# Kernel optimization log

Hardware: AMD Instinct MI355X
Metric: run time of the kernel (lower is better)

## Reference

```python
import jax, jax.numpy as jnp
import numpy as np

NUM_CLASSES = 151  # Visual Genome object classes
PRED_DIM = 51      # predicate distribution channels (50 predicates + bg)


def _conv2d(x, w, pad):
    # x: [B, Cin, H, W], w: [Cout, Cin, kh, kw]
    return jax.lax.conv_general_dilated(
        x, w, window_strides=(1, 1), padding=[(pad, pad), (pad, pad)],
        dimension_numbers=("NCHW", "OIHW", "NCHW"))


def setup_inputs() -> dict:
    key = jax.random.key(0)
    ks = jax.random.split(key, 12)
    B, N, D = 64, 80, 4096
    K = D // 4  # 1024
    s = 0.02
    return {
        "encoder_reps": jax.random.normal(ks[0], (B, N, D), jnp.float32),
        "obj_preds": jax.random.randint(ks[1], (B, N), 0, NUM_CLASSES, jnp.int32),
        "freq_table": jax.random.normal(ks[2], (NUM_CLASSES * NUM_CLASSES, PRED_DIM), jnp.float32),
        "W_comp": jax.random.normal(ks[3], (D, K), jnp.float32) * s,
        "W_ou1": jax.random.normal(ks[4], (K, K), jnp.float32) * s,
        "W_ofc": jax.random.normal(ks[5], (K, K), jnp.float32) * s,
        "W_decomp": jax.random.normal(ks[6], (K, D), jnp.float32) * s,
        "conv1": jax.random.normal(ks[7], (10, PRED_DIM, 3, 3), jnp.float32) * s,
        "conv2": jax.random.normal(ks[8], (5, 10, 3, 3), jnp.float32) * s,
        "conv3": jax.random.normal(ks[9], (1, 5, 1, 1), jnp.float32) * s,
    }


def reference(encoder_reps, obj_preds, freq_table, W_comp, W_ou1, W_ofc,
              W_decomp, conv1, conv2, conv3):
    B, N, D = encoder_reps.shape
    # obj_comp: Linear(D, D//4, bias=False) + ReLU
    comp = jax.nn.relu(jnp.einsum("bnd,dk->bnk", encoder_reps, W_comp))  # [B,N,K]
    # ou1: Linear(K, K, bias=False) + ReLU
    obj_u1 = jax.nn.relu(jnp.einsum("bnk,kj->bnj", comp, W_ou1))          # [B,N,K]
    # pairwise product indices -> freq_bias.index_with_labels (subj*C + obj)
    pair_idx = obj_preds[:, :, None] * NUM_CLASSES + obj_preds[:, None, :]  # [B,N,N]
    rel_u1 = freq_table[pair_idx]                                          # [B,N,N,51]
    # adjacency via small conv stack + sigmoid
    x = jnp.transpose(rel_u1, (0, 3, 1, 2))      # [B,51,N,N]
    x = _conv2d(x, conv1, pad=1)                 # [B,10,N,N]
    x = _conv2d(x, conv2, pad=1)                 # [B,5,N,N]
    x = _conv2d(x, conv3, pad=0)                 # [B,1,N,N]
    adj = jax.nn.sigmoid(x[:, 0])                # [B,N,N]
    # normalized Laplacian: D^-1/2 (A + I) D^-1/2
    A_hat = adj + jnp.eye(N, dtype=adj.dtype)[None]
    d = (jnp.sum(A_hat, axis=2) + 1e-5) ** (-0.5)                          # [B,N]
    L_hat = d[:, :, None] * A_hat * d[:, None, :]                          # [B,N,N]
    ofl_u = jnp.einsum("bnm,bmk->bnk", L_hat, obj_u1)                      # [B,N,K]
    # ofc_u + obj_decomp + residual
    u_m = jax.nn.relu(jnp.einsum("bnk,kj->bnj", ofl_u, W_ofc))
    decomp = jax.nn.relu(jnp.einsum("bnk,kd->bnd", u_m, W_decomp))
    return decomp + encoder_reps
```

## Files before the change

### kernel.cpp

```cpp
#include <hip/hip_runtime.h>
#include <hip/hip_bf16.h>
#include <math.h>

typedef __bf16 bf16x8 __attribute__((ext_vector_type(8)));
typedef float floatx4 __attribute__((ext_vector_type(4)));
typedef float float4v __attribute__((ext_vector_type(4)));
typedef float float2v __attribute__((ext_vector_type(2)));
typedef unsigned short ushortx4 __attribute__((ext_vector_type(4)));
typedef unsigned short ushortx8 __attribute__((ext_vector_type(8)));

__device__ __forceinline__ unsigned short f2bf(float f) {
    unsigned int u = __builtin_bit_cast(unsigned int, f);
    u += 0x7FFFu + ((u >> 16) & 1u);
    return (unsigned short)(u >> 16);
}
__device__ __forceinline__ float bf2f(unsigned short h) {
    unsigned int u = ((unsigned int)h) << 16;
    return __builtin_bit_cast(float, u);
}

__device__ __forceinline__ void gload_lds16(const void* g, void* l) {
    __builtin_amdgcn_global_load_lds(
        (const __attribute__((address_space(1))) unsigned int*)g,
        (__attribute__((address_space(3))) unsigned int*)l, 16, 0, 0);
}

__global__ __launch_bounds__(256) void cast_bf16_kernel(
    const float* __restrict__ in, unsigned short* __restrict__ out, long n8)
{
    long i = (long)blockIdx.x * 256 + threadIdx.x;
    long stride = (long)gridDim.x * 256;
    for (; i < n8; i += stride) {
        float4v a = reinterpret_cast<const float4v*>(in)[2 * i];
        float4v b = reinterpret_cast<const float4v*>(in)[2 * i + 1];
        ushortx8 h;
        #pragma unroll
        for (int q = 0; q < 4; ++q) { h[q] = f2bf(a[q]); h[4 + q] = f2bf(b[q]); }
        reinterpret_cast<ushortx8*>(out)[i] = h;
    }
}

__global__ __launch_bounds__(256) void reduce_relu_kernel(
    const unsigned short* __restrict__ p0, const unsigned short* __restrict__ p1,
    unsigned short* __restrict__ out, long n8)
{
    long i = (long)blockIdx.x * 256 + threadIdx.x;
    long stride = (long)gridDim.x * 256;
    const ushortx8* a0 = reinterpret_cast<const ushortx8*>(p0);
    const ushortx8* a1 = reinterpret_cast<const ushortx8*>(p1);
    for (; i < n8; i += stride) {
        ushortx8 x = a0[i], y = a1[i];
        ushortx8 h;
        #pragma unroll
        for (int q = 0; q < 8; ++q)
            h[q] = f2bf(fmaxf(bf2f(x[q]) + bf2f(y[q]), 0.0f));
        reinterpret_cast<ushortx8*>(out)[i] = h;
    }
}

__global__ __launch_bounds__(256) void prep_kernel(
    const float* __restrict__ w1, const float* __restrict__ w2,
    const float* __restrict__ w3, float* __restrict__ W1e,
    float* __restrict__ w23)
{
    for (int idx = threadIdx.x; idx < 4590; idx += 256) {
        int ci = idx / 90, rem = idx % 90;
        int tap = rem / 10, co = rem % 10;
        int di = tap / 3, dj = tap % 3;
        W1e[idx] = w1[((co * 51 + ci) * 3 + di) * 3 + dj];
    }
    if (threadIdx.x < 90) {
        int tap = threadIdx.x / 10, c10 = threadIdx.x % 10;
        int di = tap / 3, dj = tap % 3;
        float s = 0.f;
        #pragma unroll
        for (int c5 = 0; c5 < 5; ++c5)
            s = fmaf(w3[c5], w2[((c5 * 10 + c10) * 3 + di) * 3 + dj], s);
        w23[threadIdx.x] = s;
    }
}

__global__ __launch_bounds__(256) void fp1_kernel(
    const float* __restrict__ freq, const float* __restrict__ W1e,
    float* __restrict__ Fp1)
{
    __shared__ float W1s[4590];
    for (int idx = threadIdx.x; idx < 4590; idx += 256)
        W1s[idx] = W1e[idx];
    __syncthreads();
    int p = blockIdx.x * 256 + threadIdx.x;
    if (p >= 22801) return;
    float2v acc[45];
    #pragma unroll
    for (int t = 0; t < 45; ++t) { acc[t][0] = 0.f; acc[t][1] = 0.f; }
    const float* fr = freq + (size_t)p * 51;
    for (int ci = 0; ci < 51; ++ci) {
        float v = fr[ci];
        const float2v* wrow = reinterpret_cast<const float2v*>(&W1s[ci * 90]);
        #pragma unroll
        for (int t = 0; t < 45; ++t) {
            float2v w = wrow[t];
            acc[t][0] = fmaf(v, w[0], acc[t][0]);
            acc[t][1] = fmaf(v, w[1], acc[t][1]);
        }
    }
    float2v* out = reinterpret_cast<float2v*>(Fp1 + (size_t)p * 90);
    #pragma unroll
    for (int t = 0; t < 45; ++t) out[t] = acc[t];
}

__global__ __launch_bounds__(320) void gather_kernel(
    const int* __restrict__ preds, const float* __restrict__ Fp1,
    float* __restrict__ h1)
{
    __shared__ int pb[80];
    const int b = blockIdx.y;
    const int tid = threadIdx.x;
    if (tid < 80) pb[tid] = preds[b * 80 + tid];
    __syncthreads();
    const int i = blockIdx.x * 4 + tid / 80;
    const int j = tid % 80;
    float2v acc[5];
    #pragma unroll
    for (int q = 0; q < 5; ++q) { acc[q][0] = 0.f; acc[q][1] = 0.f; }
    #pragma unroll
    for (int di = 0; di < 3; ++di) {
        int ii = i + di - 1;
        if (ii < 0 || ii >= 80) continue;
        int pi = pb[ii] * 151;
        #pragma unroll
        for (int dj = 0; dj < 3; ++dj) {
            int jj = j + dj - 1;
            if (jj < 0 || jj >= 80) continue;
            const float2v* row = reinterpret_cast<const float2v*>(
                Fp1 + (size_t)(pi + pb[jj]) * 90 + (di * 3 + dj) * 10);
            #pragma unroll
            for (int q = 0; q < 5; ++q) {
                float2v v = row[q];
                acc[q][0] += v[0];
                acc[q][1] += v[1];
            }
        }
    }
    float2v* out = reinterpret_cast<float2v*>(
        h1 + ((size_t)b * 6400 + i * 80 + j) * 10);
    #pragma unroll
    for (int q = 0; q < 5; ++q) out[q] = acc[q];
}

__global__ __launch_bounds__(320) void conv23_kernel(
    const float* __restrict__ h1, const float* __restrict__ w23g,
    float* __restrict__ adj)
{
    __shared__ float w23s[90];
    const int tid = threadIdx.x;
    if (tid < 90) w23s[tid] = w23g[tid];
    __syncthreads();
    const int b = blockIdx.y;
    const int i = blockIdx.x * 4 + tid / 80;
    const int j = tid % 80;
    float t = 0.f;
    #pragma unroll
    for (int di = 0; di < 3; ++di) {
        int ii = i + di - 1;
        if (ii < 0 || ii >= 80) continue;
        #pragma unroll
        for (int dj = 0; dj < 3; ++dj) {
            int jj = j + dj - 1;
            if (jj < 0 || jj >= 80) continue;
            const float2v* hp = reinterpret_cast<const float2v*>(
                h1 + ((size_t)b * 6400 + ii * 80 + jj) * 10);
            const float* wp = w23s + (di * 3 + dj) * 10;
            #pragma unroll
            for (int q = 0; q < 5; ++q) {
                float2v v = hp[q];
                t = fmaf(v[0], wp[2 * q], t);
                t = fmaf(v[1], wp[2 * q + 1], t);
            }
        }
    }
    adj[(size_t)b * 6400 + i * 80 + j] = 1.0f / (1.0f + __expf(-t));
}

__global__ __launch_bounds__(128) void degree_kernel(
    const float* __restrict__ adj, float* __restrict__ deg)
{
    int b = blockIdx.x;
    int i = threadIdx.x;
    if (i >= 80) return;
    const float* row = adj + (size_t)b * 6400 + i * 80;
    float s = 1.0f + 1e-5f;
    for (int jj = 0; jj < 80; ++jj) s += row[jj];
    deg[b * 80 + i] = rsqrtf(s);
}

__global__ __launch_bounds__(256) void transpose_cast(
    const float* __restrict__ in, unsigned short* __restrict__ out,
    int R, int C)
{
    __shared__ float t[32][33];
    const int tx = threadIdx.x & 31;
    const int ty = threadIdx.x >> 5;
    const int r0 = blockIdx.y * 32, c0 = blockIdx.x * 32;
    #pragma unroll
    for (int k = 0; k < 4; ++k)
        t[ty + k * 8][tx] = in[(size_t)(r0 + ty + k * 8) * C + c0 + tx];
    __syncthreads();
    #pragma unroll
    for (int k = 0; k < 4; ++k)
        out[(size_t)(c0 + ty + k * 8) * R + r0 + tx] = f2bf(t[tx][ty + k * 8]);
}

template<int MODE>
__global__ __launch_bounds__(256) void gemm128(
    const unsigned short* __restrict__ Ap, const unsigned short* __restrict__ Bt,
    void* __restrict__ Cp, const unsigned short* __restrict__ Rb,
    unsigned short* __restrict__ P1,
    int M, int N, int lda, int kh)
{
    __shared__ __align__(16) unsigned short SS[16384];
    unsigned short* Al = SS;
    unsigned short* Bl = SS + 8192;

    const int tid  = threadIdx.x;
    const int bm   = blockIdx.x * 128;
    const int bn   = blockIdx.y * 128;
    const int k0   = blockIdx.z * kh;
    const int wave = tid >> 6;
    const int lane = tid & 63;
    const int wm   = (wave >> 1) * 64;
    const int wn   = (wave & 1) * 64;
    const int lr   = lane & 15;
    const int lo   = lane >> 4;
    const int soct = (lo ^ ((lr >> 1) & 3)) * 8;

    floatx4 acc[4][4];
    #pragma unroll
    for (int i = 0; i < 4; ++i)
        #pragma unroll
        for (int j = 0; j < 4; ++j)
            #pragma unroll
            for (int r = 0; r < 4; ++r) acc[i][j][r] = 0.0f;

    auto stage = [&](int buf, int kq) {
        #pragma unroll
        for (int it = 0; it < 2; ++it) {
            int idx = tid + it * 256;
            int r = idx >> 2, s = idx & 3;
            gload_lds16(
                &Ap[(size_t)(bm + r) * lda + kq + ((s ^ ((r >> 1) & 3)) * 8)],
                &Al[buf * 4096 + idx * 8]);
        }
        #pragma unroll
        for (int it = 0; it < 2; ++it) {
            int idx = tid + it * 256;
            int r = idx >> 2, s = idx & 3;
            gload_lds16(
                &Bt[(size_t)(bn + r) * lda + kq + ((s ^ ((r >> 1) & 3)) * 8)],
                &Bl[buf * 4096 + idx * 8]);
        }
    };

    stage(0, k0);
    __syncthreads();
    const int nt = kh >> 5;
    int cur = 0;
    for (int t = 0; t < nt; ++t) {
        if (t + 1 < nt) stage(cur ^ 1, k0 + ((t + 1) << 5));
        bf16x8 af[4], bfv[4];
        #pragma unroll
        for (int mi = 0; mi < 4; ++mi)
            af[mi] = *reinterpret_cast<const bf16x8*>(
                &Al[cur * 4096 + (wm + mi * 16 + lr) * 32 + soct]);
        #pragma unroll
        for (int ni = 0; ni < 4; ++ni)
            bfv[ni] = *reinterpret_cast<const bf16x8*>(
                &Bl[cur * 4096 + (wn + ni * 16 + lr) * 32 + soct]);
        #pragma unroll
        for (int mi = 0; mi < 4; ++mi)
            #pragma unroll
            for (int ni = 0; ni < 4; ++ni)
                acc[mi][ni] = __builtin_amdgcn_mfma_f32_16x16x32_bf16(
                    bfv[ni], af[mi], acc[mi][ni], 0, 0, 0);
        __syncthreads();
        cur ^= 1;
    }

    if (MODE == 0 || MODE == 2) {
        #pragma unroll
        for (int mi = 0; mi < 4; ++mi) {
            const int mrow = wm + mi * 16 + lr;
            const int swz = (mrow & 7) << 4;
            #pragma unroll
            for (int ni = 0; ni < 4; ++ni) {
                const int nc = wn + ni * 16 + lo * 4;
                ushortx4 v;
                #pragma unroll
                for (int rr = 0; rr < 4; ++rr)
                    v[rr] = f2bf(MODE == 0 ? fmaxf(acc[mi][ni][rr], 0.f)
                                           : acc[mi][ni][rr]);
                *reinterpret_cast<ushortx4*>(
                    (char*)SS + ((mrow * 256 + nc * 2) ^ swz)) = v;
            }
        }
        __syncthreads();
        unsigned short* dst = (MODE == 2 && blockIdx.z)
            ? P1 : (unsigned short*)Cp;
        #pragma unroll
        for (int it = 0; it < 8; ++it) {
            int idx = tid + it * 256;
            int r = idx >> 4, c = idx & 15;
            ushortx8 v = *reinterpret_cast<const ushortx8*>(
                (char*)SS + ((r * 256 + c * 16) ^ ((r & 7) << 4)));
            *reinterpret_cast<ushortx8*>(
                &dst[(size_t)(bm + r) * N + bn + c * 8]) = v;
        }
    } else {
        #pragma unroll
        for (int p = 0; p < 2; ++p) {
            if ((wave & 1) == p) {
                #pragma unroll
                for (int mi = 0; mi < 4; ++mi) {
                    const int mrow = wm + mi * 16 + lr;
                    const int swz = (mrow & 7) << 4;
                    #pragma unroll
                    for (int ni = 0; ni < 4; ++ni) {
                        const int nc = ni * 16 + lo * 4;
                        float4v v;
                        #pragma unroll
                        for (int rr = 0; rr < 4; ++rr) v[rr] = acc[mi][ni][rr];
                        *reinterpret_cast<float4v*>(
                            (char*)SS + ((mrow * 256 + nc * 4) ^ swz)) = v;
                    }
                }
            }
            __syncthreads();
            #pragma unroll
            for (int it = 0; it < 8; ++it) {
                int idx = tid + it * 256;
                int r = idx >> 4, c = idx & 15;
                float4v v = *reinterpret_cast<const float4v*>(
                    (char*)SS + ((r * 256 + c * 16) ^ ((r & 7) << 4)));
                size_t off = (size_t)(bm + r) * N + bn + p * 64 + c * 4;
                ushortx4 rv = *reinterpret_cast<const ushortx4*>(&Rb[off]);
                float4v o;
                #pragma unroll
                for (int rr = 0; rr < 4; ++rr)
                    o[rr] = fmaxf(v[rr], 0.f) + bf2f(rv[rr]);
                *reinterpret_cast<float4v*>(&((float*)Cp)[off]) = o;
            }
            if (p == 0) __syncthreads();
        }
    }
}

__global__ __launch_bounds__(256) void gemm_pipe0(
    const unsigned short* __restrict__ Ap, const unsigned short* __restrict__ Bt,
    unsigned short* __restrict__ Cp, int M, int N, int lda)
{
    __shared__ unsigned short Al[2][128 * 32];
    __shared__ unsigned short Bl[2][128 * 32];
    const int tid  = threadIdx.x;
    const int bm   = blockIdx.x * 128;
    const int bn   = blockIdx.y * 128;
    const int wave = tid >> 6;
    const int lane = tid & 63;
    const int wm   = (wave >> 1) * 64;
    const int wn   = (wave & 1) * 64;
    const int lr   = lane & 15;
    const int lk   = (lane >> 4) * 8;
    floatx4 acc[4][4];
    #pragma unroll
    for (int i = 0; i < 4; ++i)
        #pragma unroll
        for (int j = 0; j < 4; ++j)
            #pragma unroll
            for (int r = 0; r < 4; ++r) acc[i][j][r] = 0.0f;
    auto stage = [&](int buf, int kq) {
        #pragma unroll
        for (int it = 0; it < 2; ++it) {
            int idx = tid + it * 256;
            gload_lds16(&Ap[(size_t)(bm + (idx >> 2)) * lda + kq + (idx & 3) * 8],
                        &Al[buf][idx * 8]);
        }
        #pragma unroll
        for (int it = 0; it < 2; ++it) {
            int idx = tid + it * 256;
            gload_lds16(&Bt[(size_t)(bn + (idx >> 2)) * lda + kq + (idx & 3) * 8],
                        &Bl[buf][idx * 8]);
        }
    };
    stage(0, 0);
    __syncthreads();
    const int nt = lda >> 5;
    int cur = 0;
    for (int t = 0; t < nt; ++t) {
        if (t + 1 < nt) stage(cur ^ 1, (t + 1) << 5);
        bf16x8 af[4], bfv[4];
        #pragma unroll
        for (int mi = 0; mi < 4; ++mi)
            af[mi] = *reinterpret_cast<const bf16x8*>(
                &Al[cur][(wm + mi * 16 + lr) * 32 + lk]);
        #pragma unroll
        for (int ni = 0; ni < 4; ++ni)
            bfv[ni] = *reinterpret_cast<const bf16x8*>(
                &Bl[cur][(wn + ni * 16 + lr) * 32 + lk]);
        #pragma unroll
        for (int mi = 0; mi < 4; ++mi)
            #pragma unroll
            for (int ni = 0; ni < 4; ++ni)
                acc[mi][ni] = __builtin_amdgcn_mfma_f32_16x16x32_bf16(
                    af[mi], bfv[ni], acc[mi][ni], 0, 0, 0);
        __syncthreads();
        cur ^= 1;
    }
    #pragma unroll
    for (int mi = 0; mi < 4; ++mi)
        #pragma unroll
        for (int ni = 0; ni < 4; ++ni)
            #pragma unroll
            for (int r = 0; r < 4; ++r) {
                int row = bm + wm + mi * 16 + (lane >> 4) * 4 + r;
                int col = bn + wn + ni * 16 + lr;
                Cp[(size_t)row * N + col] = f2bf(fmaxf(acc[mi][ni][r], 0.f));
            }
}

__global__ __launch_bounds__(256) void gemm_f32a(
    const float* __restrict__ Ap, const unsigned short* __restrict__ Bt,
    unsigned short* __restrict__ Cp, int M, int N, int lda)
{
    __shared__ unsigned short Al[2][128 * 40];
    __shared__ unsigned short Bl[2][128 * 32];
    const int tid  = threadIdx.x;
    const int bm   = blockIdx.x * 128;
    const int bn   = blockIdx.y * 128;
    const int wave = tid >> 6;
    const int lane = tid & 63;
    const int wm   = (wave >> 1) * 64;
    const int wn   = (wave & 1) * 64;
    const int lr   = lane & 15;
    const int lk   = (lane >> 4) * 8;
    floatx4 acc[4][4];
    #pragma unroll
    for (int i = 0; i < 4; ++i)
        #pragma unroll
        for (int j = 0; j < 4; ++j)
            #pragma unroll
            for (int r = 0; r < 4; ++r) acc[i][j][r] = 0.0f;
    auto stage = [&](int buf, int k0) {
        #pragma unroll
        for (int it = 0; it < 4; ++it) {
            int idx = tid + it * 256;
            int r = idx >> 3, kc = (idx & 7) * 4;
            float4v v = *reinterpret_cast<const float4v*>(
                &Ap[(size_t)(bm + r) * lda + k0 + kc]);
            ushortx4 h;
            #pragma unroll
            for (int q = 0; q < 4; ++q) h[q] = f2bf(v[q]);
            *reinterpret_cast<ushortx4*>(&Al[buf][r * 40 + kc]) = h;
        }
        #pragma unroll
        for (int it = 0; it < 2; ++it) {
            int idx = tid + it * 256;
            gload_lds16(&Bt[(size_t)(bn + (idx >> 2)) * lda + k0 + (idx & 3) * 8],
                        &Bl[buf][idx * 8]);
        }
    };
    stage(0, 0);
    __syncthreads();
    const int nt = lda >> 5;
    int cur = 0;
    for (int t = 0; t < nt; ++t) {
        if (t + 1 < nt) stage(cur ^ 1, (t + 1) << 5);
        bf16x8 af[4], bfv[4];
        #pragma unroll
        for (int mi = 0; mi < 4; ++mi)
            af[mi] = *reinterpret_cast<const bf16x8*>(
                &Al[cur][(wm + mi * 16 + lr) * 40 + lk]);
        #pragma unroll
        for (int ni = 0; ni < 4; ++ni)
            bfv[ni] = *reinterpret_cast<const bf16x8*>(
                &Bl[cur][(wn + ni * 16 + lr) * 32 + lk]);
        #pragma unroll
        for (int mi = 0; mi < 4; ++mi)
            #pragma unroll
            for (int ni = 0; ni < 4; ++ni)
                acc[mi][ni] = __builtin_amdgcn_mfma_f32_16x16x32_bf16(
                    af[mi], bfv[ni], acc[mi][ni], 0, 0, 0);
        __syncthreads();
        cur ^= 1;
    }
    #pragma unroll
    for (int mi = 0; mi < 4; ++mi)
        #pragma unroll
        for (int ni = 0; ni < 4; ++ni)
            #pragma unroll
            for (int r = 0; r < 4; ++r) {
                int row = bm + wm + mi * 16 + (lane >> 4) * 4 + r;
                int col = bn + wn + ni * 16 + lr;
                Cp[(size_t)row * N + col] = f2bf(fmaxf(acc[mi][ni][r], 0.f));
            }
}

__global__ __launch_bounds__(256) void gemm_res_f32(
    const unsigned short* __restrict__ Ap, const unsigned short* __restrict__ Bt,
    float* __restrict__ Cp, const float* __restrict__ Rp, int M, int N, int lda)
{
    __shared__ unsigned short Al[2][128 * 32];
    __shared__ unsigned short Bl[2][128 * 32];
    const int tid  = threadIdx.x;
    const int bm   = blockIdx.x * 128;
    const int bn   = blockIdx.y * 128;
    const int wave = tid >> 6;
    const int lane = tid & 63;
    const int wm   = (wave >> 1) * 64;
    const int wn   = (wave & 1) * 64;
    const int lr   = lane & 15;
    const int lk   = (lane >> 4) * 8;
    floatx4 acc[4][4];
    #pragma unroll
    for (int i = 0; i < 4; ++i)
        #pragma unroll
        for (int j = 0; j < 4; ++j)
            #pragma unroll
            for (int r = 0; r < 4; ++r) acc[i][j][r] = 0.0f;
    auto stage = [&](int buf, int kq) {
        #pragma unroll
        for (int it = 0; it < 2; ++it) {
            int idx = tid + it * 256;
            gload_lds16(&Ap[(size_t)(bm + (idx >> 2)) * lda + kq + (idx & 3) * 8],
                        &Al[buf][idx * 8]);
        }
        #pragma unroll
        for (int it = 0; it < 2; ++it) {
            int idx = tid + it * 256;
            gload_lds16(&Bt[(size_t)(bn + (idx >> 2)) * lda + kq + (idx & 3) * 8],
                        &Bl[buf][idx * 8]);
        }
    };
    stage(0, 0);
    __syncthreads();
    const int nt = lda >> 5;
    int cur = 0;
    for (int t = 0; t < nt; ++t) {
        if (t + 1 < nt) stage(cur ^ 1, (t + 1) << 5);
        bf16x8 af[4], bfv[4];
        #pragma unroll
        for (int mi = 0; mi < 4; ++mi)
            af[mi] = *reinterpret_cast<const bf16x8*>(
                &Al[cur][(wm + mi * 16 + lr) * 32 + lk]);
        #pragma unroll
        for (int ni = 0; ni < 4; ++ni)
            bfv[ni] = *reinterpret_cast<const bf16x8*>(
                &Bl[cur][(wn + ni * 16 + lr) * 32 + lk]);
        #pragma unroll
        for (int mi = 0; mi < 4; ++mi)
            #pragma unroll
            for (int ni = 0; ni < 4; ++ni)
                acc[mi][ni] = __builtin_amdgcn_mfma_f32_16x16x32_bf16(
                    af[mi], bfv[ni], acc[mi][ni], 0, 0, 0);
        __syncthreads();
        cur ^= 1;
    }
    #pragma unroll
    for (int mi = 0; mi < 4; ++mi)
        #pragma unroll
        for (int ni = 0; ni < 4; ++ni)
            #pragma unroll
            for (int r = 0; r < 4; ++r) {
                int row = bm + wm + mi * 16 + (lane >> 4) * 4 + r;
                int col = bn + wn + ni * 16 + lr;
                size_t off = (size_t)row * N + col;
                Cp[off] = fmaxf(acc[mi][ni][r], 0.f) + Rp[off];
            }
}

__global__ __launch_bounds__(256) void laplacian_kernel(
    const float* __restrict__ adj, const float* __restrict__ deg,
    const unsigned short* __restrict__ u_in, unsigned short* __restrict__ ofl)
{
    __shared__ float wl[6400];
    __shared__ unsigned short ul[80 * 256];
    const int b   = blockIdx.y;
    const int kq  = blockIdx.x;
    const int tid = threadIdx.x;
    const int ko  = tid & 31;
    const int ngrp = tid >> 5;

    const float* ab = adj + (size_t)b * 6400;
    const float* db = deg + b * 80;
    for (int idx = tid; idx < 6400; idx += 256) {
        int n = idx / 80;
        int m = idx - n * 80;
        float w = ab[idx] + (n == m ? 1.0f : 0.0f);
        wl[idx] = w * db[m];
    }
    const unsigned short* ub = u_in + (size_t)b * 80 * 1024 + kq * 256;
    #pragma unroll
    for (int it = 0; it < 10; ++it) {
        int idx = tid + it * 256;
        int m   = idx >> 5;
        int c8  = (idx & 31) * 8;
        *reinterpret_cast<ushortx8*>(&ul[m * 256 + c8]) =
            *reinterpret_cast<const ushortx8*>(&ub[(size_t)m * 1024 + c8]);
    }
    __syncthreads();

    float acc[10][8];
    #pragma unroll
    for (int ni = 0; ni < 10; ++ni)
        #pragma unroll
        for (int q = 0; q < 8; ++q) acc[ni][q] = 0.0f;

    for (int m = 0; m < 80; ++m) {
        ushortx8 uv = *reinterpret_cast<const ushortx8*>(&ul[m * 256 + ko * 8]);
        float uf[8];
        #pragma unroll
        for (int q = 0; q < 8; ++q) uf[q] = bf2f(uv[q]);
        #pragma unroll
        for (int ni = 0; ni < 10; ++ni) {
            float wv = wl[(ngrp * 10 + ni) * 80 + m];
            #pragma unroll
            for (int q = 0; q < 8; ++q)
                acc[ni][q] = fmaf(wv, uf[q], acc[ni][q]);
        }
    }
    #pragma unroll
    for (int ni = 0; ni < 10; ++ni) {
        int n = ngrp * 10 + ni;
        float dn = db[n];
        ushortx8 o;
        #pragma unroll
        for (int q = 0; q < 8; ++q) o[q] = f2bf(acc[ni][q] * dn);
        *reinterpret_cast<ushortx8*>(
            &ofl[((size_t)(b * 80 + n)) * 1024 + kq * 256 + ko * 8]) = o;
    }
}

extern "C" void kernel_launch(void* const* d_in, const int* in_sizes, int n_in,
                              void* d_out, int out_size, void* d_ws, size_t ws_size,
                              hipStream_t stream)
{
    const float* enc   = (const float*)d_in[0];
    const int*   preds = (const int*)d_in[1];
    const float* freq  = (const float*)d_in[2];
    const float* Wc    = (const float*)d_in[3];
    const float* Wou1  = (const float*)d_in[4];
    const float* Wofc  = (const float*)d_in[5];
    const float* Wdec  = (const float*)d_in[6];
    const float* w1    = (const float*)d_in[7];
    const float* w2    = (const float*)d_in[8];
    const float* w3    = (const float*)d_in[9];

    const int M = 5120;
    const size_t SLAB = (size_t)M * 1024;
    unsigned short* comp  = (unsigned short*)d_ws;
    unsigned short* obju  = comp + SLAB;
    unsigned short* r1    = obju + SLAB;
    unsigned short* oflu  = r1;
    float*          h1    = (float*)r1;
    unsigned short* r2    = r1 + 8192000;
    unsigned short* um    = r2;
    float*          Fp1   = (float*)r2;
    unsigned short* Wcb   = r2 + SLAB;
    unsigned short* Wou1b = Wcb + (size_t)1024 * 4096;
    unsigned short* Wofcb = Wou1b + (size_t)1024 * 1024;
    unsigned short* Wdecb = Wofcb + (size_t)1024 * 1024;
    float*          W1e   = (float*)(Wdecb + (size_t)4096 * 1024);
    float*          w23   = W1e + 4590;
    float*          adj   = w23 + 90;
    float*          deg   = adj + (size_t)64 * 6400;
    unsigned short* encb  = (unsigned short*)(deg + 5120);
    const size_t need_bytes =
        ((size_t)(encb - comp) + (size_t)M * 4096) * sizeof(unsigned short);
    const bool use_encb = ws_size >= need_bytes;

    prep_kernel<<<1, 256, 0, stream>>>(w1, w2, w3, W1e, w23);
    transpose_cast<<<dim3(32, 128), 256, 0, stream>>>(Wc, Wcb, 4096, 1024);
    transpose_cast<<<dim3(32, 32), 256, 0, stream>>>(Wou1, Wou1b, 1024, 1024);
    transpose_cast<<<dim3(32, 32), 256, 0, stream>>>(Wofc, Wofcb, 1024, 1024);
    transpose_cast<<<dim3(128, 32), 256, 0, stream>>>(Wdec, Wdecb, 1024, 4096);

    fp1_kernel<<<90, 256, 0, stream>>>(freq, W1e, Fp1);
    gather_kernel<<<dim3(20, 64), 320, 0, stream>>>(preds, Fp1, h1);
    conv23_kernel<<<dim3(20, 64), 320, 0, stream>>>(h1, w23, adj);
    degree_kernel<<<64, 128, 0, stream>>>(adj, deg);

    if (use_encb) {
        cast_bf16_kernel<<<2048, 256, 0, stream>>>(enc, encb, (long)M * 4096 / 8);
        gemm128<2><<<dim3(40, 8, 2), 256, 0, stream>>>(
            encb, Wcb, r1, nullptr, r2, M, 1024, 4096, 2048);
        reduce_relu_kernel<<<2048, 256, 0, stream>>>(r1, r2, comp, SLAB / 8);
        gemm128<0><<<dim3(40, 8, 1), 256, 0, stream>>>(
            comp, Wou1b, obju, nullptr, nullptr, M, 1024, 1024, 1024);
    } else {
        gemm_f32a<<<dim3(40, 8), 256, 0, stream>>>(enc, Wcb, comp, M, 1024, 4096);
        gemm_pipe0<<<dim3(40, 8), 256, 0, stream>>>(comp, Wou1b, obju, M, 1024, 1024);
    }
    laplacian_kernel<<<dim3(4, 64), 256, 0, stream>>>(adj, deg, obju, oflu);
    if (use_encb) {
        gemm128<0><<<dim3(40, 8, 1), 256, 0, stream>>>(
            oflu, Wofcb, um, nullptr, nullptr, M, 1024, 1024, 1024);
        gemm128<1><<<dim3(40, 32, 1), 256, 0, stream>>>(
            um, Wdecb, d_out, encb, nullptr, M, 4096, 1024, 1024);
    } else {
        gemm_pipe0<<<dim3(40, 8), 256, 0, stream>>>(oflu, Wofcb, um, M, 1024, 1024);
        gemm_res_f32<<<dim3(40, 32), 256, 0, stream>>>(
            um, Wdecb, (float*)d_out, enc, M, 4096, 1024);
    }
}
```

Before: 320.4 us.

## Add triple-buffered split-phase pipelined GEMM for decomp and drop gemm_pipe0

Measured after the change: 315.0 us. Within noise of the previous version (-1.7%).

```diff
diff --git a/kernel.cpp b/kernel.cpp
--- a/kernel.cpp
+++ b/kernel.cpp
@@ -212,15 +212,15 @@
 }
 
 template<int MODE>
-__global__ __launch_bounds__(256) void gemm128(
+__global__ __launch_bounds__(256) void gemm8p(
     const unsigned short* __restrict__ Ap, const unsigned short* __restrict__ Bt,
     void* __restrict__ Cp, const unsigned short* __restrict__ Rb,
     unsigned short* __restrict__ P1,
     int M, int N, int lda, int kh)
 {
-    __shared__ __align__(16) unsigned short SS[16384];
+    __shared__ __align__(16) unsigned short SS[24576];
     unsigned short* Al = SS;
-    unsigned short* Bl = SS + 8192;
+    unsigned short* Bl = SS + 12288;
 
     const int tid  = threadIdx.x;
     const int bm   = blockIdx.x * 128;
@@ -242,7 +242,7 @@
             #pragma unroll
             for (int r = 0; r < 4; ++r) acc[i][j][r] = 0.0f;
 
-    auto stage = [&](int buf, int kq) {
+    auto stageA = [&](int buf, int kq) {
         #pragma unroll
         for (int it = 0; it < 2; ++it) {
             int idx = tid + it * 256;
@@ -251,6 +251,8 @@
                 &Ap[(size_t)(bm + r) * lda + kq + ((s ^ ((r >> 1) & 3)) * 8)],
                 &Al[buf * 4096 + idx * 8]);
         }
+    };
+    auto stageB = [&](int buf, int kq) {
         #pragma unroll
         for (int it = 0; it < 2; ++it) {
             int idx = tid + it * 256;
@@ -261,61 +263,62 @@
         }
     };
 
-    stage(0, k0);
-    __syncthreads();
     const int nt = kh >> 5;
-    int cur = 0;
+    stageA(0, k0);
+    stageB(0, k0);
+    if (nt > 1) stageA(1, k0 + 32);
+
     for (int t = 0; t < nt; ++t) {
-        if (t + 1 < nt) stage(cur ^ 1, k0 + ((t + 1) << 5));
-        bf16x8 af[4], bfv[4];
+        const int cur = t % 3;
+        if (t + 1 < nt) {
+            asm volatile("s_waitcnt vmcnt(2)" ::: "memory");
+        } else {
+            asm volatile("s_waitcnt vmcnt(0)" ::: "memory");
+        }
+        __builtin_amdgcn_s_barrier();
+        __builtin_amdgcn_sched_barrier(0);
+
+        bf16x8 af[4], bf0[2];
         #pragma unroll
         for (int mi = 0; mi < 4; ++mi)
             af[mi] = *reinterpret_cast<const bf16x8*>(
                 &Al[cur * 4096 + (wm + mi * 16 + lr) * 32 + soct]);
         #pragma unroll
-        for (int ni = 0; ni < 4; ++ni)
-            bfv[ni] = *reinterpret_cast<const bf16x8*>(
+        for (int ni = 0; ni < 2; ++ni)
+            bf0[ni] = *reinterpret_cast<const bf16x8*>(
                 &Bl[cur * 4096 + (wn + ni * 16 + lr) * 32 + soct]);
-        #pragma unroll
-        for (int mi = 0; mi < 4; ++mi)
-            #pragma unroll
-            for (int ni = 0; ni < 4; ++ni)
+        if (t + 1 < nt) stageB((t + 1) % 3, k0 + ((t + 1) << 5));
+        __builtin_amdgcn_sched_barrier(0);
+        __builtin_amdgcn_s_barrier();
+        __builtin_amdgcn_s_setprio(1);
+        #pragma unroll
+        for (int mi = 0; mi < 4; ++mi)
+            #pragma unroll
+            for (int ni = 0; ni < 2; ++ni)
                 acc[mi][ni] = __builtin_amdgcn_mfma_f32_16x16x32_bf16(
-                    bfv[ni], af[mi], acc[mi][ni], 0, 0, 0);
-        __syncthreads();
-        cur ^= 1;
-    }
-
-    if (MODE == 0 || MODE == 2) {
-        #pragma unroll
-        for (int mi = 0; mi < 4; ++mi) {
-            const int mrow = wm + mi * 16 + lr;
-            const int swz = (mrow & 7) << 4;
-            #pragma unroll
-            for (int ni = 0; ni < 4; ++ni) {
-                const int nc = wn + ni * 16 + lo * 4;
-                ushortx4 v;
-                #pragma unroll
-                for (int rr = 0; rr < 4; ++rr)
-                    v[rr] = f2bf(MODE == 0 ? fmaxf(acc[mi][ni][rr], 0.f)
-                                           : acc[mi][ni][rr]);
-                *reinterpret_cast<ushortx4*>(
-                    (char*)SS + ((mrow * 256 + nc * 2) ^ swz)) = v;
-            }
-        }
-        __syncthreads();
-        unsigned short* dst = (MODE == 2 && blockIdx.z)
-            ? P1 : (unsigned short*)Cp;
-        #pragma unroll
-        for (int it = 0; it < 8; ++it) {
-            int idx = tid + it * 256;
-            int r = idx >> 4, c = idx & 15;
-            ushortx8 v = *reinterpret_cast<const ushortx8*>(
-                (char*)SS + ((r * 256 + c * 16) ^ ((r & 7) << 4)));
-            *reinterpret_cast<ushortx8*>(
-                &dst[(size_t)(bm + r) * N + bn + c * 8]) = v;
-        }
-    } else {
+                    bf0[ni], af[mi], acc[mi][ni], 0, 0, 0);
+        __builtin_amdgcn_s_setprio(0);
+
+        bf16x8 bf1[2];
+        #pragma unroll
+        for (int ni = 0; ni < 2; ++ni)
+            bf1[ni] = *reinterpret_cast<const bf16x8*>(
+                &Bl[cur * 4096 + (wn + (ni + 2) * 16 + lr) * 32 + soct]);
+        if (t + 2 < nt) stageA((t + 2) % 3, k0 + ((t + 2) << 5));
+        __builtin_amdgcn_sched_barrier(0);
+        __builtin_amdgcn_s_barrier();
+        __builtin_amdgcn_s_setprio(1);
+        #pragma unroll
+        for (int mi = 0; mi < 4; ++mi)
+            #pragma unroll
+            for (int ni = 0; ni < 2; ++ni)
+                acc[mi][ni + 2] = __builtin_amdgcn_mfma_f32_16x16x32_bf16(
+                    bf1[ni], af[mi], acc[mi][ni + 2], 0, 0, 0);
+        __builtin_amdgcn_s_setprio(0);
+    }
+
+    __syncthreads();
+    if (MODE == 1) {
         #pragma unroll
         for (int p = 0; p < 2; ++p) {
             if ((wave & 1) == p) {
@@ -351,24 +354,59 @@
             }
             if (p == 0) __syncthreads();
         }
-    }
-}
-
-__global__ __launch_bounds__(256) void gemm_pipe0(
+    } else {
+        #pragma unroll
+        for (int mi = 0; mi < 4; ++mi) {
+            const int mrow = wm + mi * 16 + lr;
+            const int swz = (mrow & 7) << 4;
+            #pragma unroll
+            for (int ni = 0; ni < 4; ++ni) {
+                const int nc = wn + ni * 16 + lo * 4;
+                ushortx4 v;
+                #pragma unroll
+                for (int rr = 0; rr < 4; ++rr)
+                    v[rr] = f2bf(fmaxf(acc[mi][ni][rr], 0.f));
+                *reinterpret_cast<ushortx4*>(
+                    (char*)SS + ((mrow * 256 + nc * 2) ^ swz)) = v;
+            }
+        }
+        __syncthreads();
+        unsigned short* dst = (unsigned short*)Cp;
+        #pragma unroll
+        for (int it = 0; it < 8; ++it) {
+            int idx = tid + it * 256;
+            int r = idx >> 4, c = idx & 15;
+            ushortx8 v = *reinterpret_cast<const ushortx8*>(
+                (char*)SS + ((r * 256 + c * 16) ^ ((r & 7) << 4)));
+            *reinterpret_cast<ushortx8*>(
+                &dst[(size_t)(bm + r) * N + bn + c * 8]) = v;
+        }
+    }
+}
+
+template<int MODE>
+__global__ __launch_bounds__(256) void gemm128(
     const unsigned short* __restrict__ Ap, const unsigned short* __restrict__ Bt,
-    unsigned short* __restrict__ Cp, int M, int N, int lda)
-{
-    __shared__ unsigned short Al[2][128 * 32];
-    __shared__ unsigned short Bl[2][128 * 32];
+    void* __restrict__ Cp, const unsigned short* __restrict__ Rb,
+    unsigned short* __restrict__ P1,
+    int M, int N, int lda, int kh)
+{
+    __shared__ __align__(16) unsigned short SS[16384];
+    unsigned short* Al = SS;
+    unsigned short* Bl = SS + 8192;
+
     const int tid  = threadIdx.x;
     const int bm   = blockIdx.x * 128;
     const int bn   = blockIdx.y * 128;
+    const int k0   = blockIdx.z * kh;
     const int wave = tid >> 6;
     const int lane = tid & 63;
     const int wm   = (wave >> 1) * 64;
     const int wn   = (wave & 1) * 64;
     const int lr   = lane & 15;
-    const int lk   = (lane >> 4) * 8;
+    const int lo   = lane >> 4;
+    const int soct = (lo ^ ((lr >> 1) & 3)) * 8;
+
     floatx4 acc[4][4];
     #pragma unroll
     for (int i = 0; i < 4; ++i)
@@ -376,54 +414,79 @@
         for (int j = 0; j < 4; ++j)
             #pragma unroll
             for (int r = 0; r < 4; ++r) acc[i][j][r] = 0.0f;
+
     auto stage = [&](int buf, int kq) {
         #pragma unroll
         for (int it = 0; it < 2; ++it) {
             int idx = tid + it * 256;
-            gload_lds16(&Ap[(size_t)(bm + (idx >> 2)) * lda + kq + (idx & 3) * 8],
-                        &Al[buf][idx * 8]);
+            int r = idx >> 2, s = idx & 3;
+            gload_lds16(
+                &Ap[(size_t)(bm + r) * lda + kq + ((s ^ ((r >> 1) & 3)) * 8)],
+                &Al[buf * 4096 + idx * 8]);
         }
         #pragma unroll
         for (int it = 0; it < 2; ++it) {
             int idx = tid + it * 256;
-            gload_lds16(&Bt[(size_t)(bn + (idx >> 2)) * lda + kq + (idx & 3) * 8],
-                        &Bl[buf][idx * 8]);
+            int r = idx >> 2, s = idx & 3;
+            gload_lds16(
+                &Bt[(size_t)(bn + r) * lda + kq + ((s ^ ((r >> 1) & 3)) * 8)],
+                &Bl[buf * 4096 + idx * 8]);
         }
     };
-    stage(0, 0);
-    __syncthreads();
-    const int nt = lda >> 5;
+
+    stage(0, k0);
+    __syncthreads();
+    const int nt = kh >> 5;
     int cur = 0;
     for (int t = 0; t < nt; ++t) {
-        if (t + 1 < nt) stage(cur ^ 1, (t + 1) << 5);
+        if (t + 1 < nt) stage(cur ^ 1, k0 + ((t + 1) << 5));
         bf16x8 af[4], bfv[4];
         #pragma unroll
         for (int mi = 0; mi < 4; ++mi)
             af[mi] = *reinterpret_cast<const bf16x8*>(
-                &Al[cur][(wm + mi * 16 + lr) * 32 + lk]);
+                &Al[cur * 4096 + (wm + mi * 16 + lr) * 32 + soct]);
         #pragma unroll
         for (int ni = 0; ni < 4; ++ni)
             bfv[ni] = *reinterpret_cast<const bf16x8*>(
-                &Bl[cur][(wn + ni * 16 + lr) * 32 + lk]);
+                &Bl[cur * 4096 + (wn + ni * 16 + lr) * 32 + soct]);
         #pragma unroll
         for (int mi = 0; mi < 4; ++mi)
             #pragma unroll
             for (int ni = 0; ni < 4; ++ni)
                 acc[mi][ni] = __builtin_amdgcn_mfma_f32_16x16x32_bf16(
-                    af[mi], bfv[ni], acc[mi][ni], 0, 0, 0);
+                    bfv[ni], af[mi], acc[mi][ni], 0, 0, 0);
         __syncthreads();
         cur ^= 1;
     }
-    #pragma unroll
-    for (int mi = 0; mi < 4; ++mi)
-        #pragma unroll
-        for (int ni = 0; ni < 4; ++ni)
-            #pragma unroll
-            for (int r = 0; r < 4; ++r) {
-                int row = bm + wm + mi * 16 + (lane >> 4) * 4 + r;
-                int col = bn + wn + ni * 16 + lr;
-                Cp[(size_t)row * N + col] = f2bf(fmaxf(acc[mi][ni][r], 0.f));
-            }
+
+    #pragma unroll
+    for (int mi = 0; mi < 4; ++mi) {
+        const int mrow = wm + mi * 16 + lr;
+        const int swz = (mrow & 7) << 4;
+        #pragma unroll
+        for (int ni = 0; ni < 4; ++ni) {
+            const int nc = wn + ni * 16 + lo * 4;
+            ushortx4 v;
+            #pragma unroll
+            for (int rr = 0; rr < 4; ++rr)
+                v[rr] = f2bf(MODE == 0 ? fmaxf(acc[mi][ni][rr], 0.f)
+                                       : acc[mi][ni][rr]);
+            *reinterpret_cast<ushortx4*>(
+                (char*)SS + ((mrow * 256 + nc * 2) ^ swz)) = v;
+        }
+    }
+    __syncthreads();
+    unsigned short* dst = (MODE == 2 && blockIdx.z)
+        ? P1 : (unsigned short*)Cp;
+    #pragma unroll
+    for (int it = 0; it < 8; ++it) {
+        int idx = tid + it * 256;
+        int r = idx >> 4, c = idx & 15;
+        ushortx8 v = *reinterpret_cast<const ushortx8*>(
+            (char*)SS + ((r * 256 + c * 16) ^ ((r & 7) << 4)));
+        *reinterpret_cast<ushortx8*>(
+            &dst[(size_t)(bm + r) * N + bn + c * 8]) = v;
+    }
 }
 
 __global__ __launch_bounds__(256) void gemm_f32a(
@@ -696,16 +759,18 @@
             comp, Wou1b, obju, nullptr, nullptr, M, 1024, 1024, 1024);
     } else {
         gemm_f32a<<<dim3(40, 8), 256, 0, stream>>>(enc, Wcb, comp, M, 1024, 4096);
-        gemm_pipe0<<<dim3(40, 8), 256, 0, stream>>>(comp, Wou1b, obju, M, 1024, 1024);
+        gemm128<0><<<dim3(40, 8, 1), 256, 0, stream>>>(
+            comp, Wou1b, obju, nullptr, nullptr, M, 1024, 1024, 1024);
     }
     laplacian_kernel<<<dim3(4, 64), 256, 0, stream>>>(adj, deg, obju, oflu);
     if (use_encb) {
         gemm128<0><<<dim3(40, 8, 1), 256, 0, stream>>>(
             oflu, Wofcb, um, nullptr, nullptr, M, 1024, 1024, 1024);
-        gemm128<1><<<dim3(40, 32, 1), 256, 0, stream>>>(
+        gemm8p<1><<<dim3(40, 32, 1), 256, 0, stream>>>(
             um, Wdecb, d_out, encb, nullptr, M, 4096, 1024, 1024);
     } else {
-        gemm_pipe0<<<dim3(40, 8), 256, 0, stream>>>(oflu, Wofcb, um, M, 1024, 1024);
+        gemm128<0><<<dim3(40, 8, 1), 256, 0, stream>>>(
+            oflu, Wofcb, um, nullptr, nullptr, M, 1024, 1024, 1024);
         gemm_res_f32<<<dim3(40, 32), 256, 0, stream>>>(
             um, Wdecb, (float*)d_out, enc, M, 4096, 1024);
     }
```
